# Optimization experiments

Measured on AMD Instinct MI355X. Metric: run time of the kernel, lower is better.

## Reference

```python
import jax, jax.numpy as jnp
import numpy as np

N_NODES = 50000
N_EDGES = 800000
D_IN, D_HID, D_OUT = 64, 64, 1


def gcn_layer(x, src, dst, W, b):
    """GCN conv: linear transform, then degree-normalized scatter-add over edges
    (with self-loops), matching x' = D^-1/2 (A+I) D^-1/2 X W^T + b."""
    n = x.shape[0]
    h = x @ W.T + b                                   # [N, out]
    deg = jax.ops.segment_sum(jnp.ones_like(dst, dtype=h.dtype), dst,
                              num_segments=n) + 1.0   # +1 for self-loop
    inv_sqrt_deg = jax.lax.rsqrt(deg)                 # [N]
    coef = inv_sqrt_deg[src] * inv_sqrt_deg[dst]      # [E]
    msgs = h[src] * coef[:, None]                     # gather + scale
    agg = jax.ops.segment_sum(msgs, dst, num_segments=n)   # scatter-add
    agg = agg + h * (inv_sqrt_deg * inv_sqrt_deg)[:, None]  # self-loop term
    return agg


def setup_inputs() -> dict:
    key = jax.random.key(0)
    k = jax.random.split(key, 9)
    x = jax.random.normal(k[0], (N_NODES, D_IN), dtype=jnp.float32)
    edge_index = jax.random.randint(k[1], (2, N_EDGES), 0, N_NODES, dtype=jnp.int64)
    s = 0.1
    W0 = jax.random.normal(k[2], (D_HID, D_IN), dtype=jnp.float32) * s
    b0 = jnp.zeros((D_HID,), dtype=jnp.float32)
    W1 = jax.random.normal(k[3], (D_HID, D_HID), dtype=jnp.float32) * s
    b1 = jnp.zeros((D_HID,), dtype=jnp.float32)
    W2 = jax.random.normal(k[4], (D_OUT, D_HID), dtype=jnp.float32) * s
    b2 = jnp.zeros((D_OUT,), dtype=jnp.float32)
    return {"x": x, "edge_index": edge_index,
            "W0": W0, "b0": b0, "W1": W1, "b1": b1, "W2": W2, "b2": b2}


def reference(x, edge_index, W0, b0, W1, b1, W2, b2):
    src, dst = edge_index[0], edge_index[1]
    h = jax.nn.relu(gcn_layer(x, src, dst, W0, b0))
    h = jax.nn.relu(gcn_layer(h, src, dst, W1, b1))
    out = gcn_layer(h, src, dst, W2, b2)   # [N, 1] per-node logits
    return out
```

## Files before the change

kernel.cpp:

```cpp
#include <hip/hip_runtime.h>

#define N_NODES 50000
#define N_EDGES 800000
#define DMAX 64
#define ZROW N_NODES
#define NB 196
#define CELL 40
#define P1_BLKS 512
#define LIN_BLKS 3125
#define CH (50001 * 32)
#define GSUB 1563
typedef unsigned short u16;

__device__ __forceinline__ u16 f2bf(float f) {
    unsigned u = __builtin_bit_cast(unsigned, f);
    u += 0x7FFFu + ((u >> 16) & 1u);
    return (u16)(u >> 16);
}
__device__ __forceinline__ float bflo(unsigned u) {
    return __builtin_bit_cast(float, u << 16);
}
__device__ __forceinline__ float bfhi(unsigned u) {
    return __builtin_bit_cast(float, u & 0xFFFF0000u);
}

__global__ __launch_bounds__(256) void bin_lin0_k(
    const int* __restrict__ src, const int* __restrict__ dst,
    unsigned* __restrict__ payload, unsigned char* __restrict__ counts,
    const float* __restrict__ x, const float* __restrict__ W,
    const float* __restrict__ b, u16* __restrict__ hA)
{
    __shared__ float4 smem4[2009];
    int bid = blockIdx.x;
    int tid = threadIdx.x;
    if (bid < P1_BLKS) {
        unsigned* cur = (unsigned*)smem4;
        unsigned* pay = cur + NB;
        for (int i = tid; i < NB; i += 256) cur[i] = 0;
        __syncthreads();
        const int4* dst4 = (const int4*)dst;
        const int4* src4 = (const int4*)src;
        const int NQ = N_EDGES / 4;
        for (int q = bid * 256 + tid; q < NQ; q += P1_BLKS * 256) {
            int4 d = dst4[q];
            int4 s = src4[q];
#define BIN(dd, ss)                                                        \
            {                                                              \
                int bkt = (dd) >> 8;                                       \
                unsigned v = ((unsigned)(ss) << 8) | ((unsigned)(dd) & 255u); \
                int p = atomicAdd((int*)&cur[bkt], 1);                     \
                if (p < CELL) pay[bkt * CELL + p] = v;                     \
            }
            BIN(d.x, s.x) BIN(d.y, s.y) BIN(d.z, s.z) BIN(d.w, s.w)
#undef BIN
        }
        __syncthreads();
        unsigned* pg = payload + (size_t)bid * (NB * CELL);
        for (int i = tid; i < NB * CELL; i += 256) pg[i] = pay[i];
        for (int i = tid; i < NB; i += 256)
            counts[bid * NB + i] = (unsigned char)min((int)cur[i], CELL);
    } else {
        float* Ws = (float*)smem4;
        float* xs = (float*)smem4 + 64 * 68;
        int j = tid & 63, ln = tid >> 6;
        int nb = (bid - P1_BLKS) * 16;
        const float4* W4 = (const float4*)W;
#pragma unroll
        for (int i = 0; i < 4; ++i) {
            int idx4 = i * 256 + tid;
            *(float4*)&Ws[(idx4 >> 4) * 68 + (idx4 & 15) * 4] = W4[idx4];
        }
        {
            const float4* x4 = (const float4*)(x + (size_t)nb * 64);
            float4 v = x4[tid];
            *(float4*)&xs[(tid >> 4) * 68 + (tid & 15) * 4] = v;
        }
        __syncthreads();
        float a0 = b[j], a1 = a0, a2 = a0, a3 = a0;
        const float4* wp = (const float4*)&Ws[j * 68];
        const float4* p0 = (const float4*)&xs[(ln * 4 + 0) * 68];
        const float4* p1 = (const float4*)&xs[(ln * 4 + 1) * 68];
        const float4* p2 = (const float4*)&xs[(ln * 4 + 2) * 68];
        const float4* p3 = (const float4*)&xs[(ln * 4 + 3) * 68];
#pragma unroll
        for (int k4 = 0; k4 < 16; ++k4) {
            float4 w = wp[k4];
            float4 q0 = p0[k4]; a0 += w.x*q0.x + w.y*q0.y + w.z*q0.z + w.w*q0.w;
            float4 q1 = p1[k4]; a1 += w.x*q1.x + w.y*q1.y + w.z*q1.z + w.w*q1.w;
            float4 q2 = p2[k4]; a2 += w.x*q2.x + w.y*q2.y + w.z*q2.z + w.w*q2.w;
            float4 q3 = p3[k4]; a3 += w.x*q3.x + w.y*q3.y + w.z*q3.z + w.w*q3.w;
        }
        size_t cbase = (size_t)(j >> 5) * CH + (j & 31);
        hA[cbase + (size_t)(nb + ln * 4 + 0) * 32] = f2bf(a0);
        hA[cbase + (size_t)(nb + ln * 4 + 1) * 32] = f2bf(a1);
        hA[cbase + (size_t)(nb + ln * 4 + 2) * 32] = f2bf(a2);
        hA[cbase + (size_t)(nb + ln * 4 + 3) * 32] = f2bf(a3);
    }
}

__global__ __launch_bounds__(256) void place_k(
    const unsigned* __restrict__ payload, const unsigned char* __restrict__ counts,
    int* __restrict__ cnt, u16* __restrict__ csr,
    u16* __restrict__ hA, u16* __restrict__ hB)
{
    __shared__ int cur[256];
    int b = blockIdx.x, tid = threadIdx.x;
    cur[tid] = 0;
    __syncthreads();
    int base = b << 8;
    for (int sb = tid; sb < P1_BLKS; sb += 256) {
        int c = counts[sb * NB + b];
        const unsigned* cell = payload + ((size_t)sb * NB + b) * CELL;
        for (int k = 0; k < c; ++k) {
            unsigned v = cell[k];
            int loc = (int)(v & 255u);
            int slot = atomicAdd(&cur[loc], 1);
            if (slot < DMAX) csr[(size_t)(base + loc) * 64 + slot] = (u16)(v >> 8);
        }
    }
    __syncthreads();
    int n = base + tid;
    if (n < N_NODES) {
        int c = cur[tid];
        cnt[n] = c;
        int m = min(c, DMAX);
        for (int k = m; k < DMAX; ++k) csr[(size_t)n * 64 + k] = (u16)ZROW;
        float inv = rsqrtf((float)c + 1.f);
#pragma unroll
        for (int ch = 0; ch < 2; ++ch) {
            unsigned* row = (unsigned*)&hA[(size_t)ch * CH + (size_t)n * 32];
#pragma unroll
            for (int i2 = 0; i2 < 16; ++i2) {
                unsigned u = row[i2];
                float lo = bflo(u) * inv, hi = bfhi(u) * inv;
                row[i2] = ((unsigned)f2bf(hi) << 16) | f2bf(lo);
            }
        }
    }
    if (b == 0 && tid < 64) {
        int ch = tid >> 5, pos = tid & 31;
        hA[(size_t)ch * CH + (size_t)ZROW * 32 + pos] = 0;
        hB[(size_t)ch * CH + (size_t)ZROW * 32 + pos] = 0;
        csr[(size_t)ZROW * 64 + tid] = (u16)ZROW;
        if (tid == 0) cnt[ZROW] = 0;
    }
}

__device__ __forceinline__ float4 cgather(
    const u16* __restrict__ hc, const int* __restrict__ cnt,
    const u16* __restrict__ csr, u16* lds_w ,
    int nq, int lane, int oct, int r, float& invn_out, int& nmy_out)
{
#pragma unroll
    for (int i = 0; i < 4; ++i) {
        int u = i * 64 + lane;
        int row = u >> 5, col = u & 31;
        int nn = nq + row;
        nn = nn < N_NODES ? nn : ZROW;
        *(unsigned*)&lds_w[row * 68 + col * 2] = ((const unsigned*)csr)[nn * 32 + col];
    }
    int nmy = nq + oct;
    nmy_out = nmy;
    int nuse = nmy < N_NODES ? nmy : ZROW;
    int mc = cnt[nuse];
    float invn = rsqrtf((float)mc + 1.f);
    invn_out = invn;
    int m8 = (min(mc, DMAX) + 7) & ~7;
    int kmax = m8;
    kmax = max(kmax, __shfl_xor(kmax, 8, 64));
    kmax = max(kmax, __shfl_xor(kmax, 16, 64));
    kmax = max(kmax, __shfl_xor(kmax, 32, 64));
    __builtin_amdgcn_wave_barrier();
    const uint2* hp = (const uint2*)hc;
    uint2 sv = hp[(unsigned)(nuse * 8 + r)];
    float a0 = bflo(sv.x), a1 = bfhi(sv.x), a2 = bflo(sv.y), a3 = bfhi(sv.y);
    const u16* myrow = lds_w + oct * 68;
#pragma unroll 1
    for (int k = 0; k < kmax; k += 8) {
#pragma unroll
        for (int u = 0; u < 8; ++u) {
            int s = (int)myrow[k + u];
            uint2 v = hp[(unsigned)(s * 8 + r)];
            a0 += bflo(v.x); a1 += bfhi(v.x);
            a2 += bflo(v.y); a3 += bfhi(v.y);
        }
    }
    float4 o; o.x = a0; o.y = a1; o.z = a2; o.w = a3;
    return o;
}

__global__ __launch_bounds__(256) void gath1_k(const u16* __restrict__ hA,
                                               const int* __restrict__ cnt,
                                               const u16* __restrict__ csr,
                                               u16* __restrict__ rs) {
    __shared__ u16 cs[4][8][68];
    int tid = threadIdx.x, lane = tid & 63, w = tid >> 6;
    int oct = (tid >> 3) & 7, r = tid & 7;
    int set = blockIdx.x & 1, sub = blockIdx.x >> 1;
    int nq = sub * 32 + w * 8;
    const u16* hc = hA + (size_t)set * CH;
    float invn; int nmy;
    float4 a = cgather(hc, cnt, csr, &cs[w][0][0], nq, lane, oct, r, invn, nmy);
    if (nmy < N_NODES) {
        float f0 = fmaxf(a.x * invn, 0.f), f1 = fmaxf(a.y * invn, 0.f);
        float f2 = fmaxf(a.z * invn, 0.f), f3 = fmaxf(a.w * invn, 0.f);
        uint2 o;
        o.x = ((unsigned)f2bf(f1) << 16) | f2bf(f0);
        o.y = ((unsigned)f2bf(f3) << 16) | f2bf(f2);
        ((uint2*)(rs + (size_t)set * CH))[(unsigned)(nmy * 8 + r)] = o;
    }
}

__global__ __launch_bounds__(256) void mv1_k(const u16* __restrict__ rs,
                                             const int* __restrict__ cnt,
                                             const float* __restrict__ W,
                                             const float* __restrict__ b,
                                             u16* __restrict__ hB) {
    __shared__ float Ws[64 * 68];
    __shared__ float xs[16 * 68];
    int tid = threadIdx.x, j = tid & 63, ln = tid >> 6;
    int nb = blockIdx.x * 16;
    const float4* W4 = (const float4*)W;
#pragma unroll
    for (int i = 0; i < 4; ++i) {
        int idx4 = i * 256 + tid;
        *(float4*)&Ws[(idx4 >> 4) * 68 + (idx4 & 15) * 4] = W4[idx4];
    }
    {
        int t = tid >> 4, r16 = tid & 15;
        int c = r16 >> 3, g = r16 & 7;
        int n = nb + t;
        uint2 u = ((const uint2*)(rs + (size_t)c * CH))[(unsigned)(n * 8 + g)];
        float* xp = &xs[t * 68 + c * 32 + g * 4];
        xp[0] = bflo(u.x); xp[1] = bfhi(u.x);
        xp[2] = bflo(u.y); xp[3] = bfhi(u.y);
    }
    __syncthreads();
    float a0 = b[j], a1 = a0, a2 = a0, a3 = a0;
    const float4* wp = (const float4*)&Ws[j * 68];
    const float4* p0 = (const float4*)&xs[(ln * 4 + 0) * 68];
    const float4* p1 = (const float4*)&xs[(ln * 4 + 1) * 68];
    const float4* p2 = (const float4*)&xs[(ln * 4 + 2) * 68];
    const float4* p3 = (const float4*)&xs[(ln * 4 + 3) * 68];
#pragma unroll
    for (int k4 = 0; k4 < 16; ++k4) {
        float4 w = wp[k4];
        float4 q0 = p0[k4]; a0 += w.x*q0.x + w.y*q0.y + w.z*q0.z + w.w*q0.w;
        float4 q1 = p1[k4]; a1 += w.x*q1.x + w.y*q1.y + w.z*q1.z + w.w*q1.w;
        float4 q2 = p2[k4]; a2 += w.x*q2.x + w.y*q2.y + w.z*q2.z + w.w*q2.w;
        float4 q3 = p3[k4]; a3 += w.x*q3.x + w.y*q3.y + w.z*q3.z + w.w*q3.w;
    }
    size_t cbase = (size_t)(j >> 5) * CH + (j & 31);
    int n0 = nb + ln * 4;
    float i0 = rsqrtf((float)cnt[n0 + 0] + 1.f);
    float i1 = rsqrtf((float)cnt[n0 + 1] + 1.f);
    float i2 = rsqrtf((float)cnt[n0 + 2] + 1.f);
    float i3 = rsqrtf((float)cnt[n0 + 3] + 1.f);
    hB[cbase + (size_t)(n0 + 0) * 32] = f2bf(a0 * i0);
    hB[cbase + (size_t)(n0 + 1) * 32] = f2bf(a1 * i1);
    hB[cbase + (size_t)(n0 + 2) * 32] = f2bf(a2 * i2);
    hB[cbase + (size_t)(n0 + 3) * 32] = f2bf(a3 * i3);
}

__global__ __launch_bounds__(256) void gath2_k(const u16* __restrict__ hB,
                                               const int* __restrict__ cnt,
                                               const u16* __restrict__ csr,
                                               const float* __restrict__ W2,
                                               float* __restrict__ pd) {
    __shared__ u16 cs[4][8][68];
    int tid = threadIdx.x, lane = tid & 63, w = tid >> 6;
    int oct = (tid >> 3) & 7, r = tid & 7;
    int set = blockIdx.x & 1, sub = blockIdx.x >> 1;
    int nq = sub * 32 + w * 8;
    const u16* hc = hB + (size_t)set * CH;
    float invn; int nmy;
    float4 a = cgather(hc, cnt, csr, &cs[w][0][0], nq, lane, oct, r, invn, nmy);
    const float4 wv = ((const float4*)W2)[set * 8 + r];
    float p = fmaxf(a.x * invn, 0.f) * wv.x + fmaxf(a.y * invn, 0.f) * wv.y
            + fmaxf(a.z * invn, 0.f) * wv.z + fmaxf(a.w * invn, 0.f) * wv.w;
    p += __shfl_xor(p, 1, 64);
    p += __shfl_xor(p, 2, 64);
    p += __shfl_xor(p, 4, 64);
    if (r == 0 && nmy < N_NODES) pd[(size_t)set * N_NODES + nmy] = p;
}

__global__ __launch_bounds__(256) void comb_k(const float* __restrict__ pd,
                                              const int* __restrict__ cnt,
                                              const float* __restrict__ b2,
                                              float* __restrict__ h2) {
    int n = blockIdx.x * 256 + threadIdx.x;
    if (n < N_NODES) {
        float s = pd[n] + pd[N_NODES + n];
        h2[n] = (s + b2[0]) * rsqrtf((float)cnt[n] + 1.f);
    }
}

__global__ __launch_bounds__(256) void g1_k(const float* __restrict__ h2,
                                            const int* __restrict__ cnt,
                                            const u16* __restrict__ csr,
                                            float* __restrict__ out) {
    int tid = threadIdx.x, j = tid & 63, w = tid >> 6;
    int nb = blockIdx.x * 16;
#pragma unroll 1
    for (int t = 0; t < 4; ++t) {
        int n = nb + w * 4 + t;
        int mf = cnt[n];
        int m = min(mf, DMAX);
        float invn = rsqrtf((float)mf + 1.f);
        float v = 0.f;
        if (j < m) v = h2[(int)csr[(size_t)n * 64 + j]];
#pragma unroll
        for (int off = 32; off; off >>= 1) v += __shfl_xor(v, off, 64);
        if (j == 0) out[n] = (v + h2[n]) * invn;
    }
}

extern "C" void kernel_launch(void* const* d_in, const int* in_sizes, int n_in,
                              void* d_out, int out_size, void* d_ws, size_t ws_size,
                              hipStream_t stream) {
    const float* x  = (const float*)d_in[0];
    const int*   ei = (const int*)d_in[1];
    const float* W0 = (const float*)d_in[2];
    const float* b0 = (const float*)d_in[3];
    const float* W1 = (const float*)d_in[4];
    const float* b1 = (const float*)d_in[5];
    const float* W2 = (const float*)d_in[6];
    const float* b2 = (const float*)d_in[7];
    float* out = (float*)d_out;

    char* ws = (char*)d_ws;
    size_t off = 0;
    auto alloc = [&](size_t bytes) {
        void* p = ws + off;
        off = (off + bytes + 255) & ~(size_t)255;
        return p;
    };
    int*      cnt  = (int*)alloc((size_t)(N_NODES + 1) * 4);
    u16*      csr  = (u16*)alloc((size_t)(N_NODES + 1) * DMAX * 2);
    u16*      hA   = (u16*)alloc((size_t)2 * CH * 2);
    u16*      hB   = (u16*)alloc((size_t)2 * CH * 2);
    u16*      rs   = (u16*)alloc((size_t)2 * CH * 2);
    float*    pd   = (float*)alloc((size_t)2 * N_NODES * 4);
    float*    h2   = (float*)alloc((size_t)N_NODES * 4);
    unsigned* payload = (unsigned*)alloc((size_t)P1_BLKS * NB * CELL * 4);
    unsigned char* counts = (unsigned char*)alloc((size_t)P1_BLKS * NB);

    const int* src = ei;
    const int* dst = ei + N_EDGES;

    bin_lin0_k<<<P1_BLKS + LIN_BLKS, 256, 0, stream>>>(src, dst, payload, counts,
                                                       x, W0, b0, hA);
    place_k<<<NB, 256, 0, stream>>>(payload, counts, cnt, csr, hA, hB);
    gath1_k<<<GSUB * 2, 256, 0, stream>>>(hA, cnt, csr, rs);
    mv1_k<<<LIN_BLKS, 256, 0, stream>>>(rs, cnt, W1, b1, hB);
    gath2_k<<<GSUB * 2, 256, 0, stream>>>(hB, cnt, csr, W2, pd);
    comb_k<<<196, 256, 0, stream>>>(pd, cnt, b2, h2);
    g1_k<<<LIN_BLKS, 256, 0, stream>>>(h2, cnt, csr, out);
}
```

Before: 94.74 us.

## Sort nodes by degree bucket within each block to balance gather waves

place_k now builds a per-256-node permutation that orders nodes by their padded degree bucket (ceil(deg/8)) using a shared histogram and prefix sum. The gather kernels read this permutation so each wave processes 8 nodes of similar degree, which cuts the wasted iterations where kmax is the wave-wide maximum. The cost is extra LDS atomics and syncs in place_k, a perm load plus barrier in each gather block, and less contiguous node access in the gathers. The grid grows slightly to cover the padded 196*256 range, with padding entries set to ZROW.

```diff
diff --git a/kernel.cpp b/kernel.cpp
--- a/kernel.cpp
+++ b/kernel.cpp
@@ -9,7 +9,8 @@
 #define P1_BLKS 512
 #define LIN_BLKS 3125
 #define CH (50001 * 32)
-#define GSUB 1563
+#define NPERM (NB * 256)
+#define GSUB (NPERM / 32)
 typedef unsigned short u16;
 
 __device__ __forceinline__ u16 f2bf(float f) {
@@ -101,11 +102,16 @@
 __global__ __launch_bounds__(256) void place_k(
     const unsigned* __restrict__ payload, const unsigned char* __restrict__ counts,
     int* __restrict__ cnt, u16* __restrict__ csr,
-    u16* __restrict__ hA, u16* __restrict__ hB)
+    u16* __restrict__ hA, u16* __restrict__ hB, u16* __restrict__ perm)
 {
     __shared__ int cur[256];
+    __shared__ int hist[16];
+    __shared__ int cb9[16];
+    __shared__ u16 perm_l[256];
     int b = blockIdx.x, tid = threadIdx.x;
     cur[tid] = 0;
+    if (tid < 16) { hist[tid] = 0; }
+    perm_l[tid] = (u16)ZROW;
     __syncthreads();
     int base = b << 8;
     for (int sb = tid; sb < P1_BLKS; sb += 256) {
@@ -120,10 +126,13 @@
     }
     __syncthreads();
     int n = base + tid;
+    int b8 = -1;
     if (n < N_NODES) {
         int c = cur[tid];
         cnt[n] = c;
         int m = min(c, DMAX);
+        b8 = (m + 7) >> 3;
+        atomicAdd(&hist[b8], 1);
         for (int k = m; k < DMAX; ++k) csr[(size_t)n * 64 + k] = (u16)ZROW;
         float inv = rsqrtf((float)c + 1.f);
 #pragma unroll
@@ -137,6 +146,19 @@
             }
         }
     }
+    __syncthreads();
+    if (tid == 0) {
+        int s = 0;
+#pragma unroll
+        for (int i = 0; i < 9; ++i) { cb9[i] = s; s += hist[i]; hist[i] = 0; }
+    }
+    __syncthreads();
+    if (b8 >= 0) {
+        int rank = cb9[b8] + atomicAdd(&hist[b8], 1);
+        perm_l[rank] = (u16)n;
+    }
+    __syncthreads();
+    perm[base + tid] = perm_l[tid];
     if (b == 0 && tid < 64) {
         int ch = tid >> 5, pos = tid & 31;
         hA[(size_t)ch * CH + (size_t)ZROW * 32 + pos] = 0;
@@ -149,20 +171,19 @@
 __device__ __forceinline__ float4 cgather(
     const u16* __restrict__ hc, const int* __restrict__ cnt,
     const u16* __restrict__ csr, u16* lds_w ,
-    int nq, int lane, int oct, int r, float& invn_out, int& nmy_out)
+    const u16* nodes8 ,
+    int lane, int oct, int r, float& invn_out, int& nmy_out)
 {
 #pragma unroll
     for (int i = 0; i < 4; ++i) {
         int u = i * 64 + lane;
         int row = u >> 5, col = u & 31;
-        int nn = nq + row;
-        nn = nn < N_NODES ? nn : ZROW;
+        int nn = (int)nodes8[row];
         *(unsigned*)&lds_w[row * 68 + col * 2] = ((const unsigned*)csr)[nn * 32 + col];
     }
-    int nmy = nq + oct;
+    int nmy = (int)nodes8[oct];
     nmy_out = nmy;
-    int nuse = nmy < N_NODES ? nmy : ZROW;
-    int mc = cnt[nuse];
+    int mc = cnt[nmy];
     float invn = rsqrtf((float)mc + 1.f);
     invn_out = invn;
     int m8 = (min(mc, DMAX) + 7) & ~7;
@@ -172,7 +193,7 @@
     kmax = max(kmax, __shfl_xor(kmax, 32, 64));
     __builtin_amdgcn_wave_barrier();
     const uint2* hp = (const uint2*)hc;
-    uint2 sv = hp[(unsigned)(nuse * 8 + r)];
+    uint2 sv = hp[(unsigned)(nmy * 8 + r)];
     float a0 = bflo(sv.x), a1 = bfhi(sv.x), a2 = bflo(sv.y), a3 = bfhi(sv.y);
     const u16* myrow = lds_w + oct * 68;
 #pragma unroll 1
@@ -192,16 +213,19 @@
 __global__ __launch_bounds__(256) void gath1_k(const u16* __restrict__ hA,
                                                const int* __restrict__ cnt,
                                                const u16* __restrict__ csr,
+                                               const u16* __restrict__ perm,
                                                u16* __restrict__ rs) {
     __shared__ u16 cs[4][8][68];
+    __shared__ u16 pm[32];
     int tid = threadIdx.x, lane = tid & 63, w = tid >> 6;
     int oct = (tid >> 3) & 7, r = tid & 7;
     int set = blockIdx.x & 1, sub = blockIdx.x >> 1;
-    int nq = sub * 32 + w * 8;
+    if (tid < 32) pm[tid] = perm[sub * 32 + tid];
+    __syncthreads();
     const u16* hc = hA + (size_t)set * CH;
     float invn; int nmy;
-    float4 a = cgather(hc, cnt, csr, &cs[w][0][0], nq, lane, oct, r, invn, nmy);
-    if (nmy < N_NODES) {
+    float4 a = cgather(hc, cnt, csr, &cs[w][0][0], &pm[w * 8], lane, oct, r, invn, nmy);
+    if (nmy != ZROW) {
         float f0 = fmaxf(a.x * invn, 0.f), f1 = fmaxf(a.y * invn, 0.f);
         float f2 = fmaxf(a.z * invn, 0.f), f3 = fmaxf(a.w * invn, 0.f);
         uint2 o;
@@ -265,23 +289,26 @@
 __global__ __launch_bounds__(256) void gath2_k(const u16* __restrict__ hB,
                                                const int* __restrict__ cnt,
                                                const u16* __restrict__ csr,
+                                               const u16* __restrict__ perm,
                                                const float* __restrict__ W2,
                                                float* __restrict__ pd) {
     __shared__ u16 cs[4][8][68];
+    __shared__ u16 pm[32];
     int tid = threadIdx.x, lane = tid & 63, w = tid >> 6;
     int oct = (tid >> 3) & 7, r = tid & 7;
     int set = blockIdx.x & 1, sub = blockIdx.x >> 1;
-    int nq = sub * 32 + w * 8;
+    if (tid < 32) pm[tid] = perm[sub * 32 + tid];
+    __syncthreads();
     const u16* hc = hB + (size_t)set * CH;
     float invn; int nmy;
-    float4 a = cgather(hc, cnt, csr, &cs[w][0][0], nq, lane, oct, r, invn, nmy);
+    float4 a = cgather(hc, cnt, csr, &cs[w][0][0], &pm[w * 8], lane, oct, r, invn, nmy);
     const float4 wv = ((const float4*)W2)[set * 8 + r];
     float p = fmaxf(a.x * invn, 0.f) * wv.x + fmaxf(a.y * invn, 0.f) * wv.y
             + fmaxf(a.z * invn, 0.f) * wv.z + fmaxf(a.w * invn, 0.f) * wv.w;
     p += __shfl_xor(p, 1, 64);
     p += __shfl_xor(p, 2, 64);
     p += __shfl_xor(p, 4, 64);
-    if (r == 0 && nmy < N_NODES) pd[(size_t)set * N_NODES + nmy] = p;
+    if (r == 0 && nmy != ZROW) pd[(size_t)set * N_NODES + nmy] = p;
 }
 
 __global__ __launch_bounds__(256) void comb_k(const float* __restrict__ pd,
@@ -342,6 +369,7 @@
     u16*      rs   = (u16*)alloc((size_t)2 * CH * 2);
     float*    pd   = (float*)alloc((size_t)2 * N_NODES * 4);
     float*    h2   = (float*)alloc((size_t)N_NODES * 4);
+    u16*      perm = (u16*)alloc((size_t)NPERM * 2);
     unsigned* payload = (unsigned*)alloc((size_t)P1_BLKS * NB * CELL * 4);
     unsigned char* counts = (unsigned char*)alloc((size_t)P1_BLKS * NB);
 
@@ -350,10 +378,10 @@
 
     bin_lin0_k<<<P1_BLKS + LIN_BLKS, 256, 0, stream>>>(src, dst, payload, counts,
                                                        x, W0, b0, hA);
-    place_k<<<NB, 256, 0, stream>>>(payload, counts, cnt, csr, hA, hB);
-    gath1_k<<<GSUB * 2, 256, 0, stream>>>(hA, cnt, csr, rs);
+    place_k<<<NB, 256, 0, stream>>>(payload, counts, cnt, csr, hA, hB, perm);
+    gath1_k<<<GSUB * 2, 256, 0, stream>>>(hA, cnt, csr, perm, rs);
     mv1_k<<<LIN_BLKS, 256, 0, stream>>>(rs, cnt, W1, b1, hB);
-    gath2_k<<<GSUB * 2, 256, 0, stream>>>(hB, cnt, csr, W2, pd);
+    gath2_k<<<GSUB * 2, 256, 0, stream>>>(hB, cnt, csr, perm, W2, pd);
     comb_k<<<196, 256, 0, stream>>>(pd, cnt, b2, h2);
     g1_k<<<LIN_BLKS, 256, 0, stream>>>(h2, cnt, csr, out);
 }
```

Result: slower. 97.83 us (+3.3%).
